# Kernel tuning notes

Hardware: AMD Instinct MI355X
Metric: run time of the kernel (lower is better)

The kernel has to match this reference:

```python
import jax, jax.numpy as jnp
import numpy as np

B, S1, S2, D1, D2 = 4, 2048, 2048, 512, 512
H, DK, DV = 8, 64, 64


def setup_inputs() -> dict:
    key = jax.random.key(0)
    ks = jax.random.split(key, 8)
    x1 = jax.random.normal(ks[0], (B, S1, D1), dtype=jnp.float32)
    x2 = jax.random.normal(ks[1], (B, S2, D2), dtype=jnp.float32)
    x3 = jax.random.normal(ks[2], (B, S2, D2), dtype=jnp.float32)
    s = 0.02
    Wq = jax.random.normal(ks[3], (D1, H * DK), dtype=jnp.float32) * s
    Wk = jax.random.normal(ks[4], (D2, H * DK), dtype=jnp.float32) * s
    Wv = jax.random.normal(ks[5], (D2, H * DV), dtype=jnp.float32) * s
    Wo = jax.random.normal(ks[6], (H * DV, D1), dtype=jnp.float32) * s
    bo = jnp.zeros((D1,), dtype=jnp.float32)
    return {"x1": x1, "x2": x2, "x3": x3, "Wq": Wq, "Wk": Wk, "Wv": Wv, "Wo": Wo, "bo": bo}


def reference(x1, x2, x3, Wq, Wk, Wv, Wo, bo):
    b, s1, _ = x1.shape
    # project to per-head q, k, v: [B, H, S, Dh]
    q = (x1 @ Wq).reshape(b, s1, H, DK).transpose(0, 2, 1, 3)
    k = (x2 @ Wk).reshape(b, x2.shape[1], H, DK).transpose(0, 2, 1, 3)
    v = (x3 @ Wv).reshape(b, x3.shape[1], H, DV).transpose(0, 2, 1, 3)
    scores = jnp.einsum('bhqd,bhkd->bhqk', q, k) / jnp.sqrt(jnp.float32(DK))
    attn = jax.nn.softmax(scores, axis=-1)
    out = jnp.einsum('bhqk,bhkd->bhqd', attn, v)  # [B, H, S1, DV]
    out = out.transpose(0, 2, 1, 3).reshape(b, s1, H * DV)
    return out @ Wo + bo
```

## Files before the change

kernel.cpp:

```cpp
#include <hip/hip_runtime.h>

typedef __attribute__((ext_vector_type(4))) float f32x4;
typedef __attribute__((ext_vector_type(8))) __bf16 bf16x8;
typedef __attribute__((ext_vector_type(4))) __bf16 bf16x4;

#define DEVINL __device__ __forceinline__

DEVINL void gld16(const void* g, void* l) {
  __builtin_amdgcn_global_load_lds((__attribute__((address_space(1))) void*)(void*)g,
                                   (__attribute__((address_space(3))) void*)l, 16, 0, 0);
}


__global__ __launch_bounds__(256) void cvt_x(const float* x1, const float* x2, const float* x3,
                                             __bf16* o0, __bf16* o1, __bf16* o2) {
  const int z = blockIdx.y;
  const float* s = z == 0 ? x1 : z == 1 ? x2 : x3;
  __bf16* d = z == 0 ? o0 : z == 1 ? o1 : o2;
  size_t i = (size_t)blockIdx.x * 256 + threadIdx.x;
  f32x4 v = ((const f32x4*)s)[i];
  bf16x4 o;
#pragma unroll
  for (int j = 0; j < 4; ++j) o[j] = (__bf16)v[j];
  ((bf16x4*)d)[i] = o;
}

__global__ __launch_bounds__(256) void cvt_w(const float* Wq, const float* Wk, const float* Wv,
                                             const float* Wo, __bf16* WT) {
  __shared__ float t[64][65];
  const int z = blockIdx.z;
  const float* W = z == 0 ? Wq : z == 1 ? Wk : z == 2 ? Wv : Wo;
  __bf16* D = WT + (size_t)z * 512 * 512;
  const int r0 = blockIdx.x * 64, c0 = blockIdx.y * 64;
  const int tx = threadIdx.x & 63, ty = threadIdx.x >> 6;
#pragma unroll
  for (int j = 0; j < 16; ++j)
    t[ty + j * 4][tx] = W[(size_t)(r0 + ty + j * 4) * 512 + c0 + tx];
  __syncthreads();
#pragma unroll
  for (int j = 0; j < 16; ++j)
    D[(size_t)(c0 + ty + j * 4) * 512 + r0 + tx] = (__bf16)t[tx][ty + j * 4];
}


DEVINL void gemm_tile(const __bf16* A, const __bf16* Bt, int m0, int n0,
                      __bf16* As, __bf16* Bs, f32x4 acc[4][4]) {
  const int tid = threadIdx.x, lane = tid & 63, w = tid >> 6;
  const int qd = lane >> 4, r = lane & 15;
  const int wm = w & 1, wn = w >> 1;
  const char* ap[4];
  const char* bp[4];
#pragma unroll
  for (int j = 0; j < 4; ++j) {
    int c = (w * 4 + j) * 64 + lane;
    int row = c >> 3, cs = c & 7;
    int gc = cs ^ (row & 7);
    ap[j] = (const char*)A + (size_t)(m0 + row) * 1024 + gc * 16;
    bp[j] = (const char*)Bt + (size_t)(n0 + row) * 1024 + gc * 16;
  }
  int offA[4][2], offB[4][2];
#pragma unroll
  for (int t = 0; t < 4; ++t)
#pragma unroll
    for (int ks = 0; ks < 2; ++ks) {
      int m = wm * 64 + t * 16 + r;
      offA[t][ks] = m * 128 + (((ks * 4 + qd) ^ (m & 7)) * 16);
      int n = wn * 64 + t * 16 + r;
      offB[t][ks] = n * 128 + (((ks * 4 + qd) ^ (n & 7)) * 16);
    }
  char* AsC = (char*)As;
  char* BsC = (char*)Bs;
  for (int kt = 0; kt < 8; ++kt) {
    __syncthreads();
#pragma unroll
    for (int j = 0; j < 4; ++j) {
      gld16(ap[j] + kt * 128, AsC + (w * 4 + j) * 1024);
      gld16(bp[j] + kt * 128, BsC + (w * 4 + j) * 1024);
    }
    __syncthreads();
#pragma unroll
    for (int ks = 0; ks < 2; ++ks) {
      bf16x8 a[4], b[4];
#pragma unroll
      for (int t = 0; t < 4; ++t) {
        a[t] = *(const bf16x8*)(AsC + offA[t][ks]);
        b[t] = *(const bf16x8*)(BsC + offB[t][ks]);
      }
#pragma unroll
      for (int i = 0; i < 4; ++i)
#pragma unroll
        for (int j2 = 0; j2 < 4; ++j2)
          acc[i][j2] = __builtin_amdgcn_mfma_f32_16x16x32_bf16(a[i], b[j2], acc[i][j2], 0, 0, 0);
    }
  }
}

__global__ __launch_bounds__(256, 2) void gemm_proj(const __bf16* x1b, const __bf16* x2b,
                                                    const __bf16* x3b, const __bf16* WT,
                                                    __bf16* Qo, __bf16* Ko, __bf16* Vto) {
  __shared__ __align__(16) __bf16 As[128 * 64];
  __shared__ __align__(16) __bf16 Bs[128 * 64];
  const int z = blockIdx.z;
  const __bf16* A = z == 0 ? x1b : z == 1 ? x2b : x3b;
  const __bf16* Bt = WT + (size_t)z * 512 * 512;
  const int l = blockIdx.x;
  const int sidx = l >> 3;
  const int m0 = ((l & 7) * 8 + (sidx >> 2)) * 128;
  const int n0 = (sidx & 3) * 128;
  f32x4 acc[4][4] = {};
  gemm_tile(A, Bt, m0, n0, As, Bs, acc);
  const int tid = threadIdx.x, lane = tid & 63, w = tid >> 6;
  const int qd = lane >> 4, r = lane & 15, wm = w & 1, wn = w >> 1;
#pragma unroll
  for (int mt = 0; mt < 4; ++mt) {
#pragma unroll
    for (int nt = 0; nt < 4; ++nt) {
      f32x4 v = acc[mt][nt];
      int col = n0 + wn * 64 + nt * 16 + r;
      int h = col >> 6, d = col & 63;
      int mg = m0 + wm * 64 + mt * 16 + qd * 4;
      int b = mg >> 11, s = mg & 2047;
      if (z == 2) {
        bf16x4 pv;
#pragma unroll
        for (int g = 0; g < 4; ++g) pv[g] = (__bf16)v[g];
        *(bf16x4*)(Vto + ((size_t)(b * 8 + h) * 64 + d) * 2048 + s) = pv;
      } else {
        __bf16* O = (z == 0 ? Qo : Ko) + ((size_t)(b * 8 + h) * 2048 + s) * 64 + d;
#pragma unroll
        for (int g = 0; g < 4; ++g) O[(size_t)g * 64] = (__bf16)v[g];
      }
    }
  }
}

__global__ __launch_bounds__(256, 2) void gemm_out(const __bf16* Ob, const __bf16* WoT,
                                                   const float* bo, float* out) {
  __shared__ __align__(16) __bf16 As[128 * 64];
  __shared__ __align__(16) __bf16 Bs[128 * 64];
  const int l = blockIdx.x;
  const int sidx = l >> 3;
  const int m0 = ((l & 7) * 8 + (sidx >> 2)) * 128;
  const int n0 = (sidx & 3) * 128;
  f32x4 acc[4][4] = {};
  gemm_tile(Ob, WoT, m0, n0, As, Bs, acc);
  const int tid = threadIdx.x, lane = tid & 63, w = tid >> 6;
  const int qd = lane >> 4, r = lane & 15, wm = w & 1, wn = w >> 1;
#pragma unroll
  for (int nt = 0; nt < 4; ++nt) {
    int col = n0 + wn * 64 + nt * 16 + r;
    float bv = bo[col];
#pragma unroll
    for (int mt = 0; mt < 4; ++mt) {
      int mg = m0 + wm * 64 + mt * 16 + qd * 4;
#pragma unroll
      for (int g = 0; g < 4; ++g) out[(size_t)(mg + g) * 512 + col] = acc[mt][nt][g] + bv;
    }
  }
}

__global__ __launch_bounds__(256, 2) void attn(const __bf16* Q, const __bf16* K,
                                               const __bf16* Vt, __bf16* O) {
  __shared__ __align__(16) __bf16 Qs[128 * 64];
  __shared__ __align__(16) __bf16 Ks[2][64 * 64];
  __shared__ __align__(16) __bf16 Vs[2][64 * 64];
  __shared__ __align__(16) __bf16 Ps[128 * 72];
  const int tid = threadIdx.x, lane = tid & 63, w = tid >> 6;
  const int qd = lane >> 4, r = lane & 15;
  const int id = blockIdx.x;
  const int bh = (id & 7) * 4 + ((id >> 3) >> 4);
  const int q0 = ((id >> 3) & 15) * 128;
  const __bf16* Qg = Q + ((size_t)bh * 2048 + q0) * 64;
  const __bf16* Kg = K + (size_t)bh * 2048 * 64;
  const __bf16* Vg = Vt + (size_t)bh * 64 * 2048;
  char* QsC = (char*)Qs;
  char* KsC = (char*)Ks;
  char* VsC = (char*)Vs;
  char* PsC = (char*)Ps;

#pragma unroll
  for (int j = 0; j < 4; ++j) {
    int c = (w * 4 + j) * 64 + lane;
    int m = c >> 3, cs = c & 7, gc = cs ^ (m & 7);
    gld16((const char*)Qg + m * 128 + gc * 16, QsC + (w * 4 + j) * 1024);
  }
#pragma unroll
  for (int j = 0; j < 2; ++j) {
    int c = (w * 2 + j) * 64 + lane;
    int m = c >> 3, cs = c & 7, gc = cs ^ (m & 7);
    gld16((const char*)Kg + (size_t)m * 128 + gc * 16, KsC + (w * 2 + j) * 1024);
    gld16((const char*)Vg + (size_t)m * 4096 + gc * 16, VsC + (w * 2 + j) * 1024);
  }
  __syncthreads();

  bf16x8 qf[2][2];
#pragma unroll
  for (int mt = 0; mt < 2; ++mt)
#pragma unroll
    for (int ks = 0; ks < 2; ++ks) {
      int m = w * 32 + mt * 16 + r;
      qf[mt][ks] = *(const bf16x8*)(QsC + m * 128 + ((ks * 4 + qd) ^ (m & 7)) * 16);
    }

  int offKV[4][2];
#pragma unroll
  for (int t = 0; t < 4; ++t)
#pragma unroll
    for (int ks = 0; ks < 2; ++ks) {
      int n = t * 16 + r;
      offKV[t][ks] = n * 128 + ((ks * 4 + qd) ^ (n & 7)) * 16;
    }

  f32x4 oacc[2][4] = {};
  float lpart[2][4] = {};

  for (int kt = 0; kt < 32; ++kt) {
    const int cur = kt & 1;
    if (kt < 31) {
#pragma unroll
      for (int j = 0; j < 2; ++j) {
        int c = (w * 2 + j) * 64 + lane;
        int m = c >> 3, cs = c & 7, gc = cs ^ (m & 7);
        gld16((const char*)Kg + (size_t)((kt + 1) * 64 + m) * 128 + gc * 16,
              KsC + (cur ^ 1) * 8192 + (w * 2 + j) * 1024);
        gld16((const char*)Vg + (size_t)m * 4096 + (kt + 1) * 128 + gc * 16,
              VsC + (cur ^ 1) * 8192 + (w * 2 + j) * 1024);
      }
    }
    const char* Kb = KsC + cur * 8192;
    const char* Vb = VsC + cur * 8192;

    f32x4 sf[2][4] = {};
#pragma unroll
    for (int nt = 0; nt < 4; ++nt) {
      bf16x8 kf0 = *(const bf16x8*)(Kb + offKV[nt][0]);
      bf16x8 kf1 = *(const bf16x8*)(Kb + offKV[nt][1]);
#pragma unroll
      for (int mt = 0; mt < 2; ++mt) {
        sf[mt][nt] = __builtin_amdgcn_mfma_f32_16x16x32_bf16(qf[mt][0], kf0, sf[mt][nt], 0, 0, 0);
        sf[mt][nt] = __builtin_amdgcn_mfma_f32_16x16x32_bf16(qf[mt][1], kf1, sf[mt][nt], 0, 0, 0);
      }
    }
#pragma unroll
    for (int mt = 0; mt < 2; ++mt) {
      int rowbase = w * 32 + mt * 16 + qd * 4;
#pragma unroll
      for (int nt = 0; nt < 4; ++nt) {
#pragma unroll
        for (int g = 0; g < 4; ++g) {
          float p = __expf(sf[mt][nt][g] * 0.125f);
          lpart[mt][g] += p;
          Ps[(rowbase + g) * 72 + nt * 16 + r] = (__bf16)p;
        }
      }
    }
#pragma unroll
    for (int mt = 0; mt < 2; ++mt) {
      int prow = w * 32 + mt * 16 + r;
      bf16x8 pf0 = *(const bf16x8*)(PsC + prow * 144 + qd * 16);
      bf16x8 pf1 = *(const bf16x8*)(PsC + prow * 144 + 64 + qd * 16);
#pragma unroll
      for (int dvt = 0; dvt < 4; ++dvt) {
        bf16x8 vf0 = *(const bf16x8*)(Vb + offKV[dvt][0]);
        bf16x8 vf1 = *(const bf16x8*)(Vb + offKV[dvt][1]);
        oacc[mt][dvt] = __builtin_amdgcn_mfma_f32_16x16x32_bf16(pf0, vf0, oacc[mt][dvt], 0, 0, 0);
        oacc[mt][dvt] = __builtin_amdgcn_mfma_f32_16x16x32_bf16(pf1, vf1, oacc[mt][dvt], 0, 0, 0);
      }
    }
    __syncthreads();
  }

  const int b = bh >> 3, h = bh & 7;
#pragma unroll
  for (int mt = 0; mt < 2; ++mt) {
#pragma unroll
    for (int g = 0; g < 4; ++g) {
      float l = lpart[mt][g];
      l += __shfl_xor(l, 1, 64);
      l += __shfl_xor(l, 2, 64);
      l += __shfl_xor(l, 4, 64);
      l += __shfl_xor(l, 8, 64);
      float inv = 1.0f / l;
      int s = q0 + w * 32 + mt * 16 + qd * 4 + g;
#pragma unroll
      for (int dvt = 0; dvt < 4; ++dvt)
        O[((size_t)b * 2048 + s) * 512 + h * 64 + dvt * 16 + r] =
            (__bf16)(oacc[mt][dvt][g] * inv);
    }
  }
}


extern "C" void kernel_launch(void* const* d_in, const int* in_sizes, int n_in,
                              void* d_out, int out_size, void* d_ws, size_t ws_size,
                              hipStream_t stream) {
  const float* x1 = (const float*)d_in[0];
  const float* x2 = (const float*)d_in[1];
  const float* x3 = (const float*)d_in[2];
  const float* Wq = (const float*)d_in[3];
  const float* Wk = (const float*)d_in[4];
  const float* Wv = (const float*)d_in[5];
  const float* Wo = (const float*)d_in[6];
  const float* bo = (const float*)d_in[7];
  float* out = (float*)d_out;
  char* ws = (char*)d_ws;
  const size_t MB = 1ull << 20;
  __bf16* x1b = (__bf16*)(ws);
  __bf16* x2b = (__bf16*)(ws + 8 * MB);
  __bf16* x3b = (__bf16*)(ws + 16 * MB);
  __bf16* WT = (__bf16*)(ws + 24 * MB);
  __bf16* Qb = (__bf16*)(ws + 26 * MB);
  __bf16* Kb = (__bf16*)(ws + 34 * MB);
  __bf16* Vtb = (__bf16*)(ws + 42 * MB);
  __bf16* Ob = (__bf16*)(ws + 50 * MB);

  cvt_x<<<dim3(4096, 3), 256, 0, stream>>>(x1, x2, x3, x1b, x2b, x3b);
  cvt_w<<<dim3(8, 8, 4), 256, 0, stream>>>(Wq, Wk, Wv, Wo, WT);
  gemm_proj<<<dim3(256, 1, 3), 256, 0, stream>>>(x1b, x2b, x3b, WT, Qb, Kb, Vtb);
  attn<<<dim3(512), 256, 0, stream>>>(Qb, Kb, Vtb, Ob);
  gemm_out<<<dim3(256), 256, 0, stream>>>(Ob, WT + 3ull * 512 * 512, bo, out);
}
```

Before: 207.0 us.

## Split attention over KV halves, stage V transpose in LDS, shrink output GEMM tile

The attention kernel now splits each query tile's KV range into two halves, doubling the grid to 1024 blocks. Each half writes unnormalized partial outputs and row sums, and a new combine kernel adds them and normalizes. The softmax scale and log2(e) are folded into Q during projection so exp2 can be used, and the QK MFMA operands are swapped to give per-lane row sums. V's transposed store goes through LDS for coalesced 16-byte writes, and gemm_out uses 64-row tiles to launch twice as many blocks. The attention kernel drops KV double buffering to raise occupancy, which exposes load latency, and the split adds an extra kernel plus partial-buffer traffic.

```diff
diff --git a/kernel.cpp b/kernel.cpp
--- a/kernel.cpp
+++ b/kernel.cpp
@@ -98,8 +98,9 @@
 __global__ __launch_bounds__(256, 2) void gemm_proj(const __bf16* x1b, const __bf16* x2b,
                                                     const __bf16* x3b, const __bf16* WT,
                                                     __bf16* Qo, __bf16* Ko, __bf16* Vto) {
-  __shared__ __align__(16) __bf16 As[128 * 64];
-  __shared__ __align__(16) __bf16 Bs[128 * 64];
+  __shared__ __align__(16) char smem[34816];
+  __bf16* As = (__bf16*)smem;
+  __bf16* Bs = (__bf16*)(smem + 16384);
   const int z = blockIdx.z;
   const __bf16* A = z == 0 ? x1b : z == 1 ? x2b : x3b;
   const __bf16* Bt = WT + (size_t)z * 512 * 512;
@@ -111,21 +112,47 @@
   gemm_tile(A, Bt, m0, n0, As, Bs, acc);
   const int tid = threadIdx.x, lane = tid & 63, w = tid >> 6;
   const int qd = lane >> 4, r = lane & 15, wm = w & 1, wn = w >> 1;
-#pragma unroll
-  for (int mt = 0; mt < 4; ++mt) {
-#pragma unroll
-    for (int nt = 0; nt < 4; ++nt) {
-      f32x4 v = acc[mt][nt];
-      int col = n0 + wn * 64 + nt * 16 + r;
-      int h = col >> 6, d = col & 63;
-      int mg = m0 + wm * 64 + mt * 16 + qd * 4;
-      int b = mg >> 11, s = mg & 2047;
-      if (z == 2) {
-        bf16x4 pv;
-#pragma unroll
-        for (int g = 0; g < 4; ++g) pv[g] = (__bf16)v[g];
-        *(bf16x4*)(Vto + ((size_t)(b * 8 + h) * 64 + d) * 2048 + s) = pv;
-      } else {
+  const int b = m0 >> 11, sbase = m0 & 2047;
+  if (z == 2) {
+    __syncthreads();
+    char* T = smem;
+#pragma unroll
+    for (int mt = 0; mt < 4; ++mt)
+#pragma unroll
+      for (int nt = 0; nt < 4; ++nt) {
+        int dv = wn * 64 + nt * 16 + r;
+        int sl = wm * 64 + mt * 16 + qd * 4;
+        bf16x4 p4;
+#pragma unroll
+        for (int g = 0; g < 4; ++g) p4[g] = (__bf16)acc[mt][nt][g];
+        *(bf16x4*)(T + (size_t)dv * 272 + sl * 2) = p4;
+      }
+    __syncthreads();
+#pragma unroll
+    for (int p2 = 0; p2 < 2; ++p2) {
+      int dvrow = p2 * 64 + (tid >> 2);
+      int col = n0 + dvrow, h = col >> 6, d = col & 63;
+      __bf16* dst = Vto + ((size_t)(b * 8 + h) * 64 + d) * 2048 + sbase + (tid & 3) * 8;
+#pragma unroll
+      for (int j = 0; j < 4; ++j) {
+        bf16x8 vv = *(const bf16x8*)(T + (size_t)dvrow * 272 + (tid & 3) * 16 + j * 64);
+        *(bf16x8*)(dst + j * 32) = vv;
+      }
+    }
+  } else {
+    const float qscale = 0.18033688f;
+#pragma unroll
+    for (int mt = 0; mt < 4; ++mt) {
+#pragma unroll
+      for (int nt = 0; nt < 4; ++nt) {
+        f32x4 v = acc[mt][nt];
+        if (z == 0) {
+#pragma unroll
+          for (int g = 0; g < 4; ++g) v[g] *= qscale;
+        }
+        int col = n0 + wn * 64 + nt * 16 + r;
+        int h = col >> 6, d = col & 63;
+        int s = sbase + wm * 64 + mt * 16 + qd * 4;
         __bf16* O = (z == 0 ? Qo : Ko) + ((size_t)(b * 8 + h) * 2048 + s) * 64 + d;
 #pragma unroll
         for (int g = 0; g < 4; ++g) O[(size_t)g * 64] = (__bf16)v[g];
@@ -136,40 +163,92 @@
 
 __global__ __launch_bounds__(256, 2) void gemm_out(const __bf16* Ob, const __bf16* WoT,
                                                    const float* bo, float* out) {
-  __shared__ __align__(16) __bf16 As[128 * 64];
+  __shared__ __align__(16) __bf16 As[64 * 64];
   __shared__ __align__(16) __bf16 Bs[128 * 64];
-  const int l = blockIdx.x;
-  const int sidx = l >> 3;
-  const int m0 = ((l & 7) * 8 + (sidx >> 2)) * 128;
-  const int n0 = (sidx & 3) * 128;
-  f32x4 acc[4][4] = {};
-  gemm_tile(Ob, WoT, m0, n0, As, Bs, acc);
   const int tid = threadIdx.x, lane = tid & 63, w = tid >> 6;
   const int qd = lane >> 4, r = lane & 15, wm = w & 1, wn = w >> 1;
+  const int id = blockIdx.x;
+  const int rest = id >> 3;
+  const int m0 = ((id & 7) * 16 + (rest & 15)) * 64;
+  const int n0 = (rest >> 4) * 128;
+  const char* ap[2];
+  const char* bp[4];
+#pragma unroll
+  for (int j = 0; j < 2; ++j) {
+    int c = (w * 2 + j) * 64 + lane;
+    int row = c >> 3, gc = (c & 7) ^ (row & 7);
+    ap[j] = (const char*)Ob + (size_t)(m0 + row) * 1024 + gc * 16;
+  }
+#pragma unroll
+  for (int j = 0; j < 4; ++j) {
+    int c = (w * 4 + j) * 64 + lane;
+    int row = c >> 3, gc = (c & 7) ^ (row & 7);
+    bp[j] = (const char*)WoT + (size_t)(n0 + row) * 1024 + gc * 16;
+  }
+  int offA[2][2], offB[4][2];
+#pragma unroll
+  for (int ks = 0; ks < 2; ++ks) {
+#pragma unroll
+    for (int t = 0; t < 2; ++t) {
+      int m = wm * 32 + t * 16 + r;
+      offA[t][ks] = m * 128 + (((ks * 4 + qd) ^ (m & 7)) * 16);
+    }
+#pragma unroll
+    for (int t = 0; t < 4; ++t) {
+      int n = wn * 64 + t * 16 + r;
+      offB[t][ks] = n * 128 + (((ks * 4 + qd) ^ (n & 7)) * 16);
+    }
+  }
+  char* AsC = (char*)As;
+  char* BsC = (char*)Bs;
+  f32x4 acc[2][4] = {};
+  for (int kt = 0; kt < 8; ++kt) {
+    __syncthreads();
+#pragma unroll
+    for (int j = 0; j < 2; ++j) gld16(ap[j] + kt * 128, AsC + (w * 2 + j) * 1024);
+#pragma unroll
+    for (int j = 0; j < 4; ++j) gld16(bp[j] + kt * 128, BsC + (w * 4 + j) * 1024);
+    __syncthreads();
+#pragma unroll
+    for (int ks = 0; ks < 2; ++ks) {
+      bf16x8 a[2], b[4];
+#pragma unroll
+      for (int t = 0; t < 2; ++t) a[t] = *(const bf16x8*)(AsC + offA[t][ks]);
+#pragma unroll
+      for (int t = 0; t < 4; ++t) b[t] = *(const bf16x8*)(BsC + offB[t][ks]);
+#pragma unroll
+      for (int i = 0; i < 2; ++i)
+#pragma unroll
+        for (int j2 = 0; j2 < 4; ++j2)
+          acc[i][j2] = __builtin_amdgcn_mfma_f32_16x16x32_bf16(a[i], b[j2], acc[i][j2], 0, 0, 0);
+    }
+  }
 #pragma unroll
   for (int nt = 0; nt < 4; ++nt) {
     int col = n0 + wn * 64 + nt * 16 + r;
     float bv = bo[col];
 #pragma unroll
-    for (int mt = 0; mt < 4; ++mt) {
-      int mg = m0 + wm * 64 + mt * 16 + qd * 4;
+    for (int mt = 0; mt < 2; ++mt) {
+      int mg = m0 + wm * 32 + mt * 16 + qd * 4;
 #pragma unroll
       for (int g = 0; g < 4; ++g) out[(size_t)(mg + g) * 512 + col] = acc[mt][nt][g] + bv;
     }
   }
 }
 
-__global__ __launch_bounds__(256, 2) void attn(const __bf16* Q, const __bf16* K,
-                                               const __bf16* Vt, __bf16* O) {
+__global__ __launch_bounds__(256, 3) void attn(const __bf16* Q, const __bf16* K,
+                                               const __bf16* Vt, __bf16* Opart, float* Lp) {
   __shared__ __align__(16) __bf16 Qs[128 * 64];
-  __shared__ __align__(16) __bf16 Ks[2][64 * 64];
-  __shared__ __align__(16) __bf16 Vs[2][64 * 64];
+  __shared__ __align__(16) __bf16 Ks[64 * 64];
+  __shared__ __align__(16) __bf16 Vs[64 * 64];
   __shared__ __align__(16) __bf16 Ps[128 * 72];
   const int tid = threadIdx.x, lane = tid & 63, w = tid >> 6;
   const int qd = lane >> 4, r = lane & 15;
   const int id = blockIdx.x;
-  const int bh = (id & 7) * 4 + ((id >> 3) >> 4);
-  const int q0 = ((id >> 3) & 15) * 128;
+  const int rest = id >> 3;
+  const int bh = (id & 7) * 4 + (rest >> 5);
+  const int kvh = (rest >> 4) & 1;
+  const int q0 = (rest & 15) * 128;
   const __bf16* Qg = Q + ((size_t)bh * 2048 + q0) * 64;
   const __bf16* Kg = K + (size_t)bh * 2048 * 64;
   const __bf16* Vg = Vt + (size_t)bh * 64 * 2048;
@@ -181,15 +260,8 @@
 #pragma unroll
   for (int j = 0; j < 4; ++j) {
     int c = (w * 4 + j) * 64 + lane;
-    int m = c >> 3, cs = c & 7, gc = cs ^ (m & 7);
+    int m = c >> 3, gc = (c & 7) ^ (m & 7);
     gld16((const char*)Qg + m * 128 + gc * 16, QsC + (w * 4 + j) * 1024);
-  }
-#pragma unroll
-  for (int j = 0; j < 2; ++j) {
-    int c = (w * 2 + j) * 64 + lane;
-    int m = c >> 3, cs = c & 7, gc = cs ^ (m & 7);
-    gld16((const char*)Kg + (size_t)m * 128 + gc * 16, KsC + (w * 2 + j) * 1024);
-    gld16((const char*)Vg + (size_t)m * 4096 + gc * 16, VsC + (w * 2 + j) * 1024);
   }
   __syncthreads();
 
@@ -212,46 +284,44 @@
     }
 
   f32x4 oacc[2][4] = {};
-  float lpart[2][4] = {};
-
-  for (int kt = 0; kt < 32; ++kt) {
-    const int cur = kt & 1;
-    if (kt < 31) {
-#pragma unroll
-      for (int j = 0; j < 2; ++j) {
-        int c = (w * 2 + j) * 64 + lane;
-        int m = c >> 3, cs = c & 7, gc = cs ^ (m & 7);
-        gld16((const char*)Kg + (size_t)((kt + 1) * 64 + m) * 128 + gc * 16,
-              KsC + (cur ^ 1) * 8192 + (w * 2 + j) * 1024);
-        gld16((const char*)Vg + (size_t)m * 4096 + (kt + 1) * 128 + gc * 16,
-              VsC + (cur ^ 1) * 8192 + (w * 2 + j) * 1024);
-      }
-    }
-    const char* Kb = KsC + cur * 8192;
-    const char* Vb = VsC + cur * 8192;
+  float lpart[2] = {0.f, 0.f};
+
+  const int kt0 = kvh * 16;
+  for (int kt = kt0; kt < kt0 + 16; ++kt) {
+    __syncthreads();
+#pragma unroll
+    for (int j = 0; j < 2; ++j) {
+      int c = (w * 2 + j) * 64 + lane;
+      int m = c >> 3, gc = (c & 7) ^ (m & 7);
+      gld16((const char*)Kg + (size_t)(kt * 64 + m) * 128 + gc * 16, KsC + (w * 2 + j) * 1024);
+      gld16((const char*)Vg + (size_t)m * 4096 + kt * 128 + gc * 16, VsC + (w * 2 + j) * 1024);
+    }
+    __syncthreads();
 
     f32x4 sf[2][4] = {};
 #pragma unroll
     for (int nt = 0; nt < 4; ++nt) {
-      bf16x8 kf0 = *(const bf16x8*)(Kb + offKV[nt][0]);
-      bf16x8 kf1 = *(const bf16x8*)(Kb + offKV[nt][1]);
+      bf16x8 kf0 = *(const bf16x8*)(KsC + offKV[nt][0]);
+      bf16x8 kf1 = *(const bf16x8*)(KsC + offKV[nt][1]);
 #pragma unroll
       for (int mt = 0; mt < 2; ++mt) {
-        sf[mt][nt] = __builtin_amdgcn_mfma_f32_16x16x32_bf16(qf[mt][0], kf0, sf[mt][nt], 0, 0, 0);
-        sf[mt][nt] = __builtin_amdgcn_mfma_f32_16x16x32_bf16(qf[mt][1], kf1, sf[mt][nt], 0, 0, 0);
+        sf[mt][nt] = __builtin_amdgcn_mfma_f32_16x16x32_bf16(kf0, qf[mt][0], sf[mt][nt], 0, 0, 0);
+        sf[mt][nt] = __builtin_amdgcn_mfma_f32_16x16x32_bf16(kf1, qf[mt][1], sf[mt][nt], 0, 0, 0);
       }
     }
 #pragma unroll
     for (int mt = 0; mt < 2; ++mt) {
-      int rowbase = w * 32 + mt * 16 + qd * 4;
+      int q = w * 32 + mt * 16 + r;
 #pragma unroll
       for (int nt = 0; nt < 4; ++nt) {
+        bf16x4 p4;
 #pragma unroll
         for (int g = 0; g < 4; ++g) {
-          float p = __expf(sf[mt][nt][g] * 0.125f);
-          lpart[mt][g] += p;
-          Ps[(rowbase + g) * 72 + nt * 16 + r] = (__bf16)p;
+          float p = __builtin_exp2f(sf[mt][nt][g]);
+          lpart[mt] += p;
+          p4[g] = (__bf16)p;
         }
+        *(bf16x4*)(PsC + q * 144 + nt * 32 + qd * 8) = p4;
       }
     }
 #pragma unroll
@@ -261,33 +331,48 @@
       bf16x8 pf1 = *(const bf16x8*)(PsC + prow * 144 + 64 + qd * 16);
 #pragma unroll
       for (int dvt = 0; dvt < 4; ++dvt) {
-        bf16x8 vf0 = *(const bf16x8*)(Vb + offKV[dvt][0]);
-        bf16x8 vf1 = *(const bf16x8*)(Vb + offKV[dvt][1]);
+        bf16x8 vf0 = *(const bf16x8*)(VsC + offKV[dvt][0]);
+        bf16x8 vf1 = *(const bf16x8*)(VsC + offKV[dvt][1]);
         oacc[mt][dvt] = __builtin_amdgcn_mfma_f32_16x16x32_bf16(pf0, vf0, oacc[mt][dvt], 0, 0, 0);
         oacc[mt][dvt] = __builtin_amdgcn_mfma_f32_16x16x32_bf16(pf1, vf1, oacc[mt][dvt], 0, 0, 0);
       }
     }
-    __syncthreads();
-  }
-
-  const int b = bh >> 3, h = bh & 7;
+  }
+
+  const size_t pbase = (size_t)(kvh * 32 + bh) * 2048;
 #pragma unroll
   for (int mt = 0; mt < 2; ++mt) {
+    float lsum = lpart[mt];
+    lsum += __shfl_xor(lsum, 16, 64);
+    lsum += __shfl_xor(lsum, 32, 64);
+    if (lane < 16) Lp[pbase + q0 + w * 32 + mt * 16 + r] = lsum;
+  }
+  __bf16* Ob0 = Opart + pbase * 64;
+#pragma unroll
+  for (int mt = 0; mt < 2; ++mt) {
 #pragma unroll
     for (int g = 0; g < 4; ++g) {
-      float l = lpart[mt][g];
-      l += __shfl_xor(l, 1, 64);
-      l += __shfl_xor(l, 2, 64);
-      l += __shfl_xor(l, 4, 64);
-      l += __shfl_xor(l, 8, 64);
-      float inv = 1.0f / l;
       int s = q0 + w * 32 + mt * 16 + qd * 4 + g;
 #pragma unroll
       for (int dvt = 0; dvt < 4; ++dvt)
-        O[((size_t)b * 2048 + s) * 512 + h * 64 + dvt * 16 + r] =
-            (__bf16)(oacc[mt][dvt][g] * inv);
-    }
-  }
+        Ob0[(size_t)s * 64 + dvt * 16 + r] = (__bf16)oacc[mt][dvt][g];
+    }
+  }
+}
+
+__global__ __launch_bounds__(256) void combine(const __bf16* Op, const float* Lp, __bf16* Ob) {
+  int c = blockIdx.x * 256 + threadIdx.x;
+  int bhs = c >> 3;
+  int dv0 = (c & 7) * 8;
+  size_t e = (size_t)bhs * 64 + dv0;
+  bf16x8 a = *(const bf16x8*)(Op + e);
+  bf16x8 b2 = *(const bf16x8*)(Op + ((size_t)32 * 2048 * 64) + e);
+  float inv = 1.0f / (Lp[bhs] + Lp[bhs + 65536]);
+  int bh = bhs >> 11, s = bhs & 2047, b = bh >> 3, h = bh & 7;
+  bf16x8 o;
+#pragma unroll
+  for (int j = 0; j < 8; ++j) o[j] = (__bf16)(((float)a[j] + (float)b2[j]) * inv);
+  *(bf16x8*)(Ob + ((size_t)(b * 2048 + s)) * 512 + h * 64 + dv0) = o;
 }
 
 
@@ -313,10 +398,13 @@
   __bf16* Kb = (__bf16*)(ws + 34 * MB);
   __bf16* Vtb = (__bf16*)(ws + 42 * MB);
   __bf16* Ob = (__bf16*)(ws + 50 * MB);
+  __bf16* Opart = (__bf16*)(ws + 58 * MB);
+  float* Lp = (float*)(ws + 74 * MB);
 
   cvt_x<<<dim3(4096, 3), 256, 0, stream>>>(x1, x2, x3, x1b, x2b, x3b);
   cvt_w<<<dim3(8, 8, 4), 256, 0, stream>>>(Wq, Wk, Wv, Wo, WT);
   gemm_proj<<<dim3(256, 1, 3), 256, 0, stream>>>(x1b, x2b, x3b, WT, Qb, Kb, Vtb);
-  attn<<<dim3(512), 256, 0, stream>>>(Qb, Kb, Vtb, Ob);
-  gemm_out<<<dim3(256), 256, 0, stream>>>(Ob, WT + 3ull * 512 * 512, bo, out);
-}
+  attn<<<dim3(1024), 256, 0, stream>>>(Qb, Kb, Vtb, Opart, Lp);
+  combine<<<dim3(2048), 256, 0, stream>>>(Opart, Lp, Ob);
+  gemm_out<<<dim3(512), 256, 0, stream>>>(Ob, WT + 3ull * 512 * 512, bo, out);
+}
```

New measurement: 201.5 us. -2.7%, faster.
